# Performance work log

Hardware: AMD Instinct MI355X
Metric: run time of the kernel (lower is better)

## Reference

```python
import jax, jax.numpy as jnp
import numpy as np

N = 100000
E = 1600000
F_IN = 256   # 4 * 64 after concat
H = 128

def _glorot(key, shape):
    fan_in, fan_out = shape
    lim = jnp.sqrt(6.0 / (fan_in + fan_out))
    return jax.random.uniform(key, shape, jnp.float32, -lim, lim)

def setup_inputs() -> dict:
    key = jax.random.key(0)
    ks = jax.random.split(key, 32)
    inp = {
        'x': jax.random.normal(ks[0], (N, 64), jnp.float32),
        'diff': jax.random.normal(ks[1], (N, 64), jnp.float32),
        'rec_prev': jax.random.normal(ks[2], (N, 64), jnp.float32),
        'hidden_prev': jax.random.normal(ks[3], (N, 64), jnp.float32),
        'edge_index': jax.random.randint(ks[4], (2, E), 0, N, jnp.int64),
    }
    dims = [(F_IN, H), (H, H), (H, H), (H, 1)]
    for i, (din, dout) in enumerate(dims):
        inp[f'Wl{i}'] = _glorot(ks[5 + 3 * i], (din, dout))  # neighbor (aggr) weight
        inp[f'Wr{i}'] = _glorot(ks[6 + 3 * i], (din, dout))  # root weight
        inp[f'b{i}'] = jnp.zeros((dout,), jnp.float32)
    return inp

def _sage_conv(h, src, dst, Wl, Wr, b):
    # mean aggregation of source-node features at destination nodes (PyG SAGEConv)
    msg_sum = jax.ops.segment_sum(h[src], dst, num_segments=N)        # [N, F]
    cnt = jax.ops.segment_sum(jnp.ones((src.shape[0],), h.dtype), dst, num_segments=N)
    mean = msg_sum / jnp.maximum(cnt, 1.0)[:, None]
    return mean @ Wl + h @ Wr + b

def reference(x, diff, rec_prev, hidden_prev, edge_index,
              Wl0, Wr0, b0, Wl1, Wr1, b1, Wl2, Wr2, b2, Wl3, Wr3, b3):
    src, dst = edge_index[0], edge_index[1]
    h = jnp.concatenate([x, diff, rec_prev, hidden_prev], axis=1)  # [N, 256]
    params = [(Wl0, Wr0, b0), (Wl1, Wr1, b1), (Wl2, Wr2, b2), (Wl3, Wr3, b3)]
    h = _sage_conv(h, src, dst, *params[0])
    for Wl, Wr, b in params[1:]:
        h = jax.nn.relu(h)
        h = _sage_conv(h, src, dst, Wl, Wr, b)
    out = jax.nn.sigmoid(h)          # [N, 1]
    lwp_util = jnp.mean(out)
    return out, lwp_util
```

## Files before the change

kernel.cpp:

```cpp
#include <hip/hip_runtime.h>
#include <hip/hip_bf16.h>

#define NN 100000
#define EE 1600000
#define HH 128
#define NB 391
#define CAP 5120
#define GB 1563

typedef short bf16x8 __attribute__((ext_vector_type(8)));
typedef short bf16x4 __attribute__((ext_vector_type(4)));
typedef float f32x4  __attribute__((ext_vector_type(4)));

__device__ inline short f2bf(float v) {
    __hip_bfloat16 b = __float2bfloat16(v);
    return *reinterpret_cast<short*>(&b);
}

typedef __attribute__((address_space(1))) void gvoid_t;
typedef __attribute__((address_space(3))) void svoid_t;
__device__ __forceinline__ void gload16(const void* g, void* l) {
    __builtin_amdgcn_global_load_lds((gvoid_t*)g, (svoid_t*)l, 16, 0, 0);
}

__device__ __forceinline__ void ld_fence() { asm volatile("" ::: "memory"); }

template <int N>
__device__ __forceinline__ void wait_vm_bar() {
    if constexpr (N == 0)
        asm volatile("s_waitcnt vmcnt(0)\n\ts_barrier" ::: "memory");
    else if constexpr (N == 8)
        asm volatile("s_waitcnt vmcnt(8)\n\ts_barrier" ::: "memory");
    else if constexpr (N == 12)
        asm volatile("s_waitcnt vmcnt(12)\n\ts_barrier" ::: "memory");
    else if constexpr (N == 16)
        asm volatile("s_waitcnt vmcnt(16)\n\ts_barrier" ::: "memory");
    else if constexpr (N == 18)
        asm volatile("s_waitcnt vmcnt(18)\n\ts_barrier" ::: "memory");
    else if constexpr (N == 20)
        asm volatile("s_waitcnt vmcnt(20)\n\ts_barrier" ::: "memory");
    else
        static_assert(N == 0 || N == 8 || N == 12 || N == 16 || N == 18 || N == 20,
                      "bad N");
}
__device__ __forceinline__ void barrier_only() {
    asm volatile("s_barrier" ::: "memory");
}

__global__ __launch_bounds__(1024) void prep_kernel(
    const float* __restrict__ Wl0, const float* __restrict__ Wr0,
    const float* __restrict__ Wl1, const float* __restrict__ Wr1,
    const float* __restrict__ Wl2, const float* __restrict__ Wr2,
    __hip_bfloat16* __restrict__ WT0, __hip_bfloat16* __restrict__ WT1,
    __hip_bfloat16* __restrict__ WT2, int* __restrict__ bcur) {
    const int t = threadIdx.x;
    if (blockIdx.x == 128) {
        if (t < NB) bcur[t] = 0;
        return;
    }
    int id = blockIdx.x * 1024 + t;
    if (id < 65536) {
        int k = id & 255, n = id >> 8;
        float v = (n < 128) ? Wl0[(size_t)k * 128 + n]
                            : Wr0[(size_t)k * 128 + (n - 128)];
        WT0[(size_t)n * 256 + k] = __float2bfloat16(v);
    } else {
        id -= 65536;
        int layer = id >> 15;
        int u = id & 32767;
        int k = u & 127, n = u >> 7;
        const float* Wl = layer ? Wl2 : Wl1;
        const float* Wr = layer ? Wr2 : Wr1;
        __hip_bfloat16* WT = layer ? WT2 : WT1;
        float v = (n < 128) ? Wl[(size_t)k * 128 + n]
                            : Wr[(size_t)k * 128 + (n - 128)];
        WT[(size_t)n * 128 + k] = __float2bfloat16(v);
    }
}

#define EW 264
template <int K, bool FIRST>
__device__ __forceinline__ void gemm_body(
    short* __restrict__ lsh, int bid,
    const __hip_bfloat16* hin,
    const float* __restrict__ x0, const float* __restrict__ x1,
    const float* __restrict__ x2, const float* __restrict__ x3,
    const __hip_bfloat16* __restrict__ wt, const float* __restrict__ bias,
    __hip_bfloat16* zout, __hip_bfloat16* __restrict__ rout) {
    const int t    = threadIdx.x;
    const int w    = t >> 6;
    const int lane = t & 63;
    const int quad = lane >> 4;
    const int l16  = lane & 15;
    const int n0   = bid * 64;

    constexpr int BUFB = FIRST ? 16384 : 8192;
    char* const lc = (char*)lsh;

    const __hip_bfloat16* afeat[4];
#pragma unroll
    for (int ft = 0; ft < 4; ++ft)
        afeat[ft] = wt + (size_t)(w * 64 + ft * 16 + l16) * K + quad * 8;

    f32x4 acc[4][4];
#pragma unroll
    for (int ft = 0; ft < 4; ++ft)
#pragma unroll
        for (int nt = 0; nt < 4; ++nt)
            acc[ft][nt] = (f32x4){0.f, 0.f, 0.f, 0.f};

    bf16x8 wreg[2][8];

    auto loadW = [&](int p, int pb) {
#pragma unroll
        for (int kcl = 0; kcl < 2; ++kcl)
#pragma unroll
            for (int ft = 0; ft < 4; ++ft)
                wreg[pb][kcl * 4 + ft] =
                    *(const bf16x8*)(afeat[ft] + (p * 2 + kcl) * 32);
    };

    auto stage = [&](int p, int bb) {
        char* lb = lc + bb * BUFB;
        if constexpr (FIRST) {
            const float* sp = (p == 0) ? x0 : (p == 1) ? x1 : (p == 2) ? x2 : x3;
#pragma unroll
            for (int i = 0; i < 4; ++i) {
                const int j   = w * 4 + i;
                const int row = j * 4 + (lane >> 4);
                int rg = n0 + row; if (rg > NN - 1) rg = NN - 1;
                const int colb = ((lane & 15) * 16) ^ ((row & 15) << 4);
                gload16((const char*)sp + (size_t)rg * 256 + colb, lb + j * 1024);
            }
        } else {
#pragma unroll
            for (int i = 0; i < 2; ++i) {
                const int j   = w * 2 + i;
                const int row = j * 8 + (lane >> 3);
                int rg = n0 + row; if (rg > NN - 1) rg = NN - 1;
                const int colb = ((lane & 7) * 16) ^ ((row & 7) << 4);
                gload16((const char*)hin + (size_t)rg * 256 + p * 128 + colb,
                        lb + j * 1024);
            }
        }
    };

    auto compute = [&](int s, int bb, int pb) {
        const char* lb = lc + bb * BUFB;
#pragma unroll
        for (int kcl = 0; kcl < 2; ++kcl) {
#pragma unroll
            for (int nt = 0; nt < 4; ++nt) {
                const int row = nt * 16 + l16;
                bf16x8 b;
                if constexpr (FIRST) {
                    const int sw = (row & 15) << 4;
                    const int B0 = kcl * 128 + quad * 32;
                    const char* rb = lb + row * 256;
                    const f32x4 lo = *(const f32x4*)(rb + ((B0) ^ sw));
                    const f32x4 hi = *(const f32x4*)(rb + ((B0 + 16) ^ sw));
                    b[0] = f2bf(lo[0]); b[1] = f2bf(lo[1]);
                    b[2] = f2bf(lo[2]); b[3] = f2bf(lo[3]);
                    b[4] = f2bf(hi[0]); b[5] = f2bf(hi[1]);
                    b[6] = f2bf(hi[2]); b[7] = f2bf(hi[3]);
                } else {
                    const int sw = (row & 7) << 4;
                    const int B0 = kcl * 64 + quad * 16;
                    b = *(const bf16x8*)(lb + row * 128 + (B0 ^ sw));
                }
#pragma unroll
                for (int ft = 0; ft < 4; ++ft)
                    acc[ft][nt] = __builtin_amdgcn_mfma_f32_16x16x32_bf16(
                        wreg[pb][kcl * 4 + ft], b, acc[ft][nt], 0, 0, 0);
            }
        }
    };

    if constexpr (FIRST) {
        stage(0, 0); ld_fence();
        stage(1, 1); ld_fence();
        loadW(0, 0); ld_fence();
        wait_vm_bar<12>(); loadW(1, 1); stage(2, 2); compute(0, 0, 0); barrier_only();
        wait_vm_bar<20>(); loadW(2, 0); stage(3, 0); compute(1, 1, 1); barrier_only();
        wait_vm_bar<12>(); loadW(3, 1);              compute(2, 2, 0); barrier_only();
        wait_vm_bar<8>();                            compute(3, 0, 1); barrier_only();
    } else {
        stage(0, 0); ld_fence();
        stage(1, 1); ld_fence();
        loadW(0, 0); loadW(1, 1);
        wait_vm_bar<18>(); compute(0, 0, 0); barrier_only();
        wait_vm_bar<16>(); compute(1, 1, 1); barrier_only();
    }

#pragma unroll
    for (int ft = 0; ft < 4; ++ft) {
        const int fb = ft * 16 + quad * 4;
        float4 bv = make_float4(0.f, 0.f, 0.f, 0.f);
        if (w >= 2) bv = *(const float4*)&bias[(w - 2) * 64 + fb];
        const int cbase = (w & 1) * 64 + ((w >= 2) ? 128 : 0);
#pragma unroll
        for (int nt = 0; nt < 4; ++nt) {
            const f32x4 a = acc[ft][nt];
            bf16x4 p;
            p[0] = f2bf(a[0] + bv.x); p[1] = f2bf(a[1] + bv.y);
            p[2] = f2bf(a[2] + bv.z); p[3] = f2bf(a[3] + bv.w);
            *(bf16x4*)&lsh[(nt * 16 + l16) * EW + cbase + fb] = p;
        }
    }
    __syncthreads();
#pragma unroll
    for (int u = 0; u < 8; ++u) {
        const int id  = u * 256 + t;
        const int row = id >> 5, ch = (id & 31) * 8;
        const int nd  = n0 + row;
        if (nd < NN) {
            const bf16x8 v = *(const bf16x8*)&lsh[row * EW + ch];
            if (ch < 128) *(bf16x8*)&zout[(size_t)nd * HH + ch] = v;
            else          *(bf16x8*)&rout[(size_t)nd * HH + (ch - 128)] = v;
        }
    }
}

template <int K, bool FIRST>
__global__ __launch_bounds__(256) void gemm_kernel(
    const __hip_bfloat16* hin,
    const float* __restrict__ x0, const float* __restrict__ x1,
    const float* __restrict__ x2, const float* __restrict__ x3,
    const __hip_bfloat16* __restrict__ wt, const float* __restrict__ bias,
    __hip_bfloat16* zout, __hip_bfloat16* __restrict__ rout) {
    __shared__ short lsh[16896];
    gemm_body<K, FIRST>(lsh, blockIdx.x, hin, x0, x1, x2, x3, wt, bias, zout, rout);
}

__global__ __launch_bounds__(256) void gemm0_scatter_kernel(
    const float* __restrict__ x0, const float* __restrict__ x1,
    const float* __restrict__ x2, const float* __restrict__ x3,
    const __hip_bfloat16* __restrict__ wt, const float* __restrict__ bias,
    __hip_bfloat16* __restrict__ zout, __hip_bfloat16* __restrict__ rout,
    const int* __restrict__ srcv, const int* __restrict__ dstv,
    int* __restrict__ bcur, int* __restrict__ pairs) {
    __shared__ short lsh[24576];
    const int t = threadIdx.x;

    if (blockIdx.x >= NB) {
        gemm_body<256, true>(lsh, blockIdx.x - NB, nullptr, x0, x1, x2, x3,
                             wt, bias, zout, rout);
        return;
    }

    int* hist = (int*)lsh;
    int* base = hist + NB;
    for (int j = t; j < NB; j += 256) hist[j] = 0;
    __syncthreads();

    const int e0 = blockIdx.x * 4096;
    int s[16], d[16];
#pragma unroll
    for (int u = 0; u < 16; ++u) {
        const int e = e0 + u * 256 + t;
        if (e < EE) {
            s[u] = srcv[e]; d[u] = dstv[e];
            atomicAdd(&hist[d[u] >> 8], 1);
        } else {
            d[u] = -1;
        }
    }
    __syncthreads();

    for (int j = t; j < NB; j += 256)
        base[j] = hist[j] ? atomicAdd(&bcur[j], hist[j]) : 0;
    __syncthreads();
    for (int j = t; j < NB; j += 256) hist[j] = base[j];
    __syncthreads();

#pragma unroll
    for (int u = 0; u < 16; ++u)
        if (d[u] >= 0) {
            const int b   = d[u] >> 8;
            const int pos = atomicAdd(&hist[b], 1);
            if (pos < CAP) pairs[b * CAP + pos] = (s[u] << 8) | (d[u] & 255);
        }
}

__global__ __launch_bounds__(256) void finalize_kernel(
    const int* __restrict__ bcur, const int* __restrict__ pairs,
    int* __restrict__ csr, int* __restrict__ beg, int* __restrict__ eend,
    float* __restrict__ inv) {
    __shared__ int cnt[256];
    __shared__ int scn[256];
    __shared__ int cur[256];
    const int b = blockIdx.x, t = threadIdx.x;
    int m = bcur[b];
    if (m > CAP) m = CAP;

    cnt[t] = 0;
    __syncthreads();
    for (int e = t; e < m; e += 256)
        atomicAdd(&cnt[pairs[b * CAP + e] & 255], 1);
    __syncthreads();

    const int v = cnt[t];
    scn[t] = v;
    __syncthreads();
    for (int st = 1; st < 256; st <<= 1) {
        int tv = (t >= st) ? scn[t - st] : 0;
        __syncthreads();
        scn[t] += tv;
        __syncthreads();
    }
    const int myStart = scn[t] - v;
    cur[t] = myStart;
    __syncthreads();

    for (int e = t; e < m; e += 256) {
        const int pk  = pairs[b * CAP + e];
        const int pos = atomicAdd(&cur[pk & 255], 1);
        csr[b * CAP + pos] = pk >> 8;
    }

    const int node = b * 256 + t;
    if (node < NN) {
        beg[node]  = b * CAP + myStart;
        eend[node] = b * CAP + myStart + v;
        inv[node]  = 1.0f / fmaxf((float)v, 1.0f);
    }
}

template <bool LAST>
__global__ __launch_bounds__(256) void aggregate_kernel(
    const __hip_bfloat16* __restrict__ z, __hip_bfloat16* __restrict__ rio,
    const int* __restrict__ beg, const int* __restrict__ eend,
    const int* __restrict__ csr, const float* __restrict__ inv,
    const float* __restrict__ Wl3, const float* __restrict__ Wr3,
    const float* __restrict__ b3, float* __restrict__ z3,
    float* __restrict__ r3) {
    const int i    = (blockIdx.x * 256 + threadIdx.x) >> 6;
    const int lane = threadIdx.x & 63;
    const int g    = lane >> 4;
    const int l16  = lane & 15;
    if (i >= NN) return;
    const int b0 = beg[i], e0 = eend[i];

    float acc[8];
#pragma unroll
    for (int j = 0; j < 8; ++j) acc[j] = 0.f;

    int e = b0 + g;
    for (; e + 12 < e0; e += 16) {
        const int s0 = csr[e];
        const int s1 = csr[e + 4];
        const int s2 = csr[e + 8];
        const int s3 = csr[e + 12];
        const bf16x8 z0 = *(const bf16x8*)&z[(size_t)s0 * HH + l16 * 8];
        const bf16x8 z1 = *(const bf16x8*)&z[(size_t)s1 * HH + l16 * 8];
        const bf16x8 z2 = *(const bf16x8*)&z[(size_t)s2 * HH + l16 * 8];
        const bf16x8 z3v = *(const bf16x8*)&z[(size_t)s3 * HH + l16 * 8];
        const __hip_bfloat162* p0 = (const __hip_bfloat162*)&z0;
        const __hip_bfloat162* p1 = (const __hip_bfloat162*)&z1;
        const __hip_bfloat162* p2 = (const __hip_bfloat162*)&z2;
        const __hip_bfloat162* p3 = (const __hip_bfloat162*)&z3v;
#pragma unroll
        for (int j = 0; j < 4; ++j) {
            acc[2 * j]     += __bfloat162float(p0[j].x) + __bfloat162float(p1[j].x)
                            + __bfloat162float(p2[j].x) + __bfloat162float(p3[j].x);
            acc[2 * j + 1] += __bfloat162float(p0[j].y) + __bfloat162float(p1[j].y)
                            + __bfloat162float(p2[j].y) + __bfloat162float(p3[j].y);
        }
    }
    for (; e < e0; e += 4) {
        const int s0 = csr[e];
        const bf16x8 z0 = *(const bf16x8*)&z[(size_t)s0 * HH + l16 * 8];
        const __hip_bfloat162* p0 = (const __hip_bfloat162*)&z0;
#pragma unroll
        for (int j = 0; j < 4; ++j) {
            acc[2 * j]     += __bfloat162float(p0[j].x);
            acc[2 * j + 1] += __bfloat162float(p0[j].y);
        }
    }

#pragma unroll
    for (int j = 0; j < 8; ++j) {
        acc[j] += __shfl_xor(acc[j], 16, 64);
        acc[j] += __shfl_xor(acc[j], 32, 64);
    }

    const float iv = inv[i];
    const int   f  = l16 * 8 + g * 2;
    const __hip_bfloat162 rv = *(const __hip_bfloat162*)&rio[(size_t)i * HH + f];
    const float ox = fmaxf(acc[g * 2]     * iv + __bfloat162float(rv.x), 0.f);
    const float oy = fmaxf(acc[g * 2 + 1] * iv + __bfloat162float(rv.y), 0.f);

    if (!LAST) {
        __hip_bfloat162 o;
        o.x = __float2bfloat16(ox);
        o.y = __float2bfloat16(oy);
        *(__hip_bfloat162*)&rio[(size_t)i * HH + f] = o;
    } else {
        const float2 wl = *(const float2*)&Wl3[f];
        const float2 wr = *(const float2*)&Wr3[f];
        float al = ox * wl.x + oy * wl.y;
        float ar = ox * wr.x + oy * wr.y;
#pragma unroll
        for (int m = 32; m; m >>= 1) {
            al += __shfl_xor(al, m, 64);
            ar += __shfl_xor(ar, m, 64);
        }
        if (lane == 0) {
            z3[i] = al;
            r3[i] = ar + b3[0];
        }
    }
}

__global__ __launch_bounds__(256) void final_kernel(
    const float* __restrict__ z3, const float* __restrict__ r3,
    const int* __restrict__ beg, const int* __restrict__ eend,
    const int* __restrict__ csr, const float* __restrict__ inv,
    float* __restrict__ out, float* __restrict__ partial) {
    __shared__ float red[4];
    const int i    = (blockIdx.x * 256 + threadIdx.x) >> 6;
    const int lane = threadIdx.x & 63;
    const int w    = threadIdx.x >> 6;
    float v = 0.f;
    if (i < NN) {
        const int b0 = beg[i], e0 = eend[i];
        float a = 0.f;
        for (int e = b0 + lane; e < e0; e += 64) a += z3[csr[e]];
#pragma unroll
        for (int m = 32; m; m >>= 1) a += __shfl_xor(a, m, 64);
        const float pre = a * inv[i] + r3[i];
        const float s = 1.f / (1.f + __expf(-pre));
        if (lane == 0) { out[i] = s; v = s; }
    }
    if (lane == 0) red[w] = v;
    __syncthreads();
    if (threadIdx.x == 0)
        partial[blockIdx.x] = red[0] + red[1] + red[2] + red[3];
}

__global__ __launch_bounds__(256) void mean_kernel(const float* __restrict__ partial,
                                                   int nb, float* __restrict__ out) {
    __shared__ float lds[256];
    float s = 0.f;
    for (int i = threadIdx.x; i < nb; i += 256) s += partial[i];
    lds[threadIdx.x] = s;
    __syncthreads();
    for (int st = 128; st; st >>= 1) {
        if (threadIdx.x < st) lds[threadIdx.x] += lds[threadIdx.x + st];
        __syncthreads();
    }
    if (threadIdx.x == 0) out[NN] = lds[0] / (float)NN;
}

extern "C" void kernel_launch(void* const* d_in, const int* in_sizes, int n_in,
                              void* d_out, int out_size, void* d_ws, size_t ws_size,
                              hipStream_t stream) {
    const float* x    = (const float*)d_in[0];
    const float* diff = (const float*)d_in[1];
    const float* rec  = (const float*)d_in[2];
    const float* hid  = (const float*)d_in[3];
    const int* edge   = (const int*)d_in[4];
    const int* esrc = edge;
    const int* edst = edge + EE;
    const float* Wl0 = (const float*)d_in[5];
    const float* Wr0 = (const float*)d_in[6];
    const float* b0  = (const float*)d_in[7];
    const float* Wl1 = (const float*)d_in[8];
    const float* Wr1 = (const float*)d_in[9];
    const float* b1  = (const float*)d_in[10];
    const float* Wl2 = (const float*)d_in[11];
    const float* Wr2 = (const float*)d_in[12];
    const float* b2  = (const float*)d_in[13];
    const float* Wl3 = (const float*)d_in[14];
    const float* Wr3 = (const float*)d_in[15];
    const float* b3  = (const float*)d_in[16];
    float* out = (float*)d_out;

    char* w = (char*)d_ws;
    auto alloc = [&](size_t bytes) -> void* {
        void* p = (void*)w;
        w += (bytes + 255) & ~(size_t)255;
        return p;
    };
    __hip_bfloat16* bufA = (__hip_bfloat16*)alloc((size_t)NN * HH * 2);
    __hip_bfloat16* bufB = (__hip_bfloat16*)alloc((size_t)NN * HH * 2);
    __hip_bfloat16* WT0  = (__hip_bfloat16*)alloc((size_t)256 * 256 * 2);
    __hip_bfloat16* WT1  = (__hip_bfloat16*)alloc((size_t)256 * 128 * 2);
    __hip_bfloat16* WT2  = (__hip_bfloat16*)alloc((size_t)256 * 128 * 2);
    int*   pairs   = (int*)alloc((size_t)NB * CAP * 4);
    int*   csr     = (int*)alloc((size_t)NB * CAP * 4);
    int*   bcur    = (int*)alloc((size_t)512 * 4);
    int*   beg     = (int*)alloc((size_t)NN * 4);
    int*   eend    = (int*)alloc((size_t)NN * 4);
    float* inv     = (float*)alloc((size_t)NN * 4);
    float* z3      = (float*)alloc((size_t)NN * 4);
    float* r3      = (float*)alloc((size_t)NN * 4);
    float* partial = (float*)alloc((size_t)25000 * 4);

    const int WB = (NN + 3) / 4;

    prep_kernel<<<129, 1024, 0, stream>>>(Wl0, Wr0, Wl1, Wr1, Wl2, Wr2,
                                          WT0, WT1, WT2, bcur);

    gemm0_scatter_kernel<<<GB + NB, 256, 0, stream>>>(
        x, diff, rec, hid, WT0, b0, bufA, bufB, esrc, edst, bcur, pairs);

    finalize_kernel<<<NB, 256, 0, stream>>>(bcur, pairs, csr, beg, eend, inv);

    aggregate_kernel<false><<<WB, 256, 0, stream>>>(bufA, bufB, beg, eend, csr, inv,
                                                    nullptr, nullptr, nullptr,
                                                    nullptr, nullptr);

    gemm_kernel<128, false><<<GB, 256, 0, stream>>>(bufB, nullptr, nullptr, nullptr, nullptr,
                                                    WT1, b1, bufB, bufA);
    aggregate_kernel<false><<<WB, 256, 0, stream>>>(bufB, bufA, beg, eend, csr, inv,
                                                    nullptr, nullptr, nullptr,
                                                    nullptr, nullptr);

    gemm_kernel<128, false><<<GB, 256, 0, stream>>>(bufA, nullptr, nullptr, nullptr, nullptr,
                                                    WT2, b2, bufA, bufB);
    aggregate_kernel<true><<<WB, 256, 0, stream>>>(bufA, bufB, beg, eend, csr, inv,
                                                   Wl3, Wr3, b3, z3, r3);

    final_kernel<<<WB, 256, 0, stream>>>(z3, r3, beg, eend, csr, inv, out, partial);
    mean_kernel<<<1, 256, 0, stream>>>(partial, WB, out);
}
```

Baseline: 499.1 us.

## Use fewer, larger scatter blocks that bucket many edge chunks each

The edge-bucketing part of the fused gemm0/scatter kernel now runs on 64 blocks instead of 391, and each block loops over a contiguous range of 25000 edges in chunks of 4096. The goal is fewer global atomics on the bucket cursors, since each block reserves one range per bucket for a much larger edge set. In exchange, each scatter block does far more serial work and reads dst twice, once for the histogram pass and once for the write pass. This can lengthen the critical path if these blocks finish after the gemm blocks.

```diff
diff --git a/kernel.cpp b/kernel.cpp
--- a/kernel.cpp
+++ b/kernel.cpp
@@ -7,6 +7,8 @@
 #define NB 391
 #define CAP 5120
 #define GB 1563
+#define SB 64
+#define EPB (EE / SB)
 
 typedef short bf16x8 __attribute__((ext_vector_type(8)));
 typedef short bf16x4 __attribute__((ext_vector_type(4)));
@@ -146,7 +148,7 @@
     };
 
     auto compute = [&](int s, int bb, int pb) {
-        const char* lb = lc + bb * BUFB;
+        const char* lb = lc + (bb)*BUFB;
 #pragma unroll
         for (int kcl = 0; kcl < 2; ++kcl) {
 #pragma unroll
@@ -242,8 +244,8 @@
     __shared__ short lsh[24576];
     const int t = threadIdx.x;
 
-    if (blockIdx.x >= NB) {
-        gemm_body<256, true>(lsh, blockIdx.x - NB, nullptr, x0, x1, x2, x3,
+    if (blockIdx.x >= SB) {
+        gemm_body<256, true>(lsh, blockIdx.x - SB, nullptr, x0, x1, x2, x3,
                              wt, bias, zout, rout);
         return;
     }
@@ -253,17 +255,19 @@
     for (int j = t; j < NB; j += 256) hist[j] = 0;
     __syncthreads();
 
-    const int e0 = blockIdx.x * 4096;
-    int s[16], d[16];
-#pragma unroll
-    for (int u = 0; u < 16; ++u) {
-        const int e = e0 + u * 256 + t;
-        if (e < EE) {
-            s[u] = srcv[e]; d[u] = dstv[e];
-            atomicAdd(&hist[d[u] >> 8], 1);
-        } else {
-            d[u] = -1;
-        }
+    const int e0   = blockIdx.x * EPB;
+    const int eend_ = e0 + EPB;
+
+    for (int be = e0; be < eend_; be += 4096) {
+        int d[16];
+#pragma unroll
+        for (int u = 0; u < 16; ++u) {
+            const int e = be + u * 256 + t;
+            d[u] = (e < eend_) ? dstv[e] : -1;
+        }
+#pragma unroll
+        for (int u = 0; u < 16; ++u)
+            if (d[u] >= 0) atomicAdd(&hist[d[u] >> 8], 1);
     }
     __syncthreads();
 
@@ -273,13 +277,22 @@
     for (int j = t; j < NB; j += 256) hist[j] = base[j];
     __syncthreads();
 
-#pragma unroll
-    for (int u = 0; u < 16; ++u)
-        if (d[u] >= 0) {
-            const int b   = d[u] >> 8;
-            const int pos = atomicAdd(&hist[b], 1);
-            if (pos < CAP) pairs[b * CAP + pos] = (s[u] << 8) | (d[u] & 255);
-        }
+    for (int be = e0; be < eend_; be += 4096) {
+        int s[16], d[16];
+#pragma unroll
+        for (int u = 0; u < 16; ++u) {
+            const int e = be + u * 256 + t;
+            if (e < eend_) { s[u] = srcv[e]; d[u] = dstv[e]; }
+            else d[u] = -1;
+        }
+#pragma unroll
+        for (int u = 0; u < 16; ++u)
+            if (d[u] >= 0) {
+                const int b   = d[u] >> 8;
+                const int pos = atomicAdd(&hist[b], 1);
+                if (pos < CAP) pairs[b * CAP + pos] = (s[u] << 8) | (d[u] & 255);
+            }
+    }
 }
 
 __global__ __launch_bounds__(256) void finalize_kernel(
@@ -502,7 +515,7 @@
     prep_kernel<<<129, 1024, 0, stream>>>(Wl0, Wr0, Wl1, Wr1, Wl2, Wr2,
                                           WT0, WT1, WT2, bcur);
 
-    gemm0_scatter_kernel<<<GB + NB, 256, 0, stream>>>(
+    gemm0_scatter_kernel<<<GB + SB, 256, 0, stream>>>(
         x, diff, rec, hid, WT0, b0, bufA, bufB, esrc, edst, bcur, pairs);
 
     finalize_kernel<<<NB, 256, 0, stream>>>(bcur, pairs, csr, beg, eend, inv);
```

Result: no change. 497.7 us (-0.3%).
